# Kernel tuning notes

Measured on AMD Instinct MI355X. Metric: run time of the kernel, lower is better.

Reference implementation:

```python
import jax, jax.numpy as jnp
import numpy as np

EPS = 1e-10


def setup_inputs() -> dict:
    key = jax.random.key(0)
    k1, k2 = jax.random.split(key)
    b, p, c = 8192, 512, 1000
    x = jax.random.normal(k1, (b, p), dtype=jnp.float32)
    means = jax.random.normal(k2, (c, p), dtype=jnp.float32)
    return {"x": x, "means": means}


def reference(x, means):
    # scale factor: L2 norm of the first class mean (np.linalg.norm(mean_logits_np[0]))
    scale = jnp.sqrt(jnp.sum(means[0] ** 2))
    # L2-normalize x along feature dim, then rescale to ||means[0]||
    xn = x / (jnp.linalg.norm(x, axis=1, keepdims=True) + EPS) * scale
    # logits = -||xn - mu_c||^2, expanded as -(||xn||^2 - 2 xn.mu + ||mu||^2)
    # avoids materializing the (b, num_classes, p) intermediate of the original
    x_sq = jnp.sum(xn * xn, axis=1, keepdims=True)          # (b, 1)
    m_sq = jnp.sum(means * means, axis=1)                   # (c,)
    cross = jnp.einsum('bp,cp->bc', xn, means)              # (b, c)
    logits = -(x_sq - 2.0 * cross + m_sq[None, :])
    return logits
```

## Files before the change

kernel.cpp:

```cpp
#include <hip/hip_runtime.h>
#include <hip/hip_bf16.h>
#include <stdint.h>

typedef __bf16 bf16x8 __attribute__((ext_vector_type(8)));
typedef float  f32x4  __attribute__((ext_vector_type(4)));
typedef __attribute__((address_space(1))) const void* gptr_t;
typedef __attribute__((address_space(3))) void*       sptr_t;

#define B_ROWS 8192
#define C_CLS  1000
#define C_PAD  1024
#define P_DIM  512
#define EPS    1e-10f

#define WS_MEANS_BF 0
#define WS_MSQ      1048576
#define WS_XN_BF    1052672
#define WS_XSQ      9441280

__device__ __forceinline__ float dot8(float4 a, float4 b) {
    return a.x * a.x + a.y * a.y + a.z * a.z + a.w * a.w
         + b.x * b.x + b.y * b.y + b.z * b.z + b.w * b.w;
}

__global__ __launch_bounds__(256) void prep_k(const float* __restrict__ x,
                                              const float* __restrict__ means,
                                              __hip_bfloat16* __restrict__ means_bf,
                                              float* __restrict__ m_sq,
                                              __hip_bfloat16* __restrict__ xn_bf,
                                              float* __restrict__ x_sq) {
    const int w = threadIdx.x >> 6;
    const int l = threadIdx.x & 63;
    const int bid = blockIdx.x;

    if (bid < B_ROWS / 4) {
        const int row = bid * 4 + w;
        const float4* m0 = (const float4*)means;
        float4 ma = m0[l * 2];
        float4 mb = m0[l * 2 + 1];
        float ms = dot8(ma, mb);
        const float4* xr = (const float4*)(x + (size_t)row * P_DIM);
        float4 a = xr[l * 2];
        float4 b = xr[l * 2 + 1];
        float s = dot8(a, b);
        #pragma unroll
        for (int off = 32; off > 0; off >>= 1) {
            ms += __shfl_down(ms, off);
            s  += __shfl_down(s, off);
        }
        ms = __shfl(ms, 0);
        s  = __shfl(s, 0);
        float scale = sqrtf(ms);
        float norm  = sqrtf(s);
        float sc    = scale / (norm + EPS);
        alignas(16) __hip_bfloat16 tmp[8];
        tmp[0] = __float2bfloat16(a.x * sc); tmp[1] = __float2bfloat16(a.y * sc);
        tmp[2] = __float2bfloat16(a.z * sc); tmp[3] = __float2bfloat16(a.w * sc);
        tmp[4] = __float2bfloat16(b.x * sc); tmp[5] = __float2bfloat16(b.y * sc);
        tmp[6] = __float2bfloat16(b.z * sc); tmp[7] = __float2bfloat16(b.w * sc);
        *(uint4*)(xn_bf + (size_t)row * P_DIM + l * 8) = *(const uint4*)tmp;
        if (l == 0) {
            float sn = sc * norm;
            x_sq[row] = sn * sn;
        }
    } else {
        const int c = (bid - B_ROWS / 4) * 4 + w;
        if (c < C_CLS) {
            const float4* mr = (const float4*)(means + (size_t)c * P_DIM);
            float4 a = mr[l * 2];
            float4 b = mr[l * 2 + 1];
            float s = dot8(a, b);
            alignas(16) __hip_bfloat16 tmp[8];
            tmp[0] = __float2bfloat16(a.x); tmp[1] = __float2bfloat16(a.y);
            tmp[2] = __float2bfloat16(a.z); tmp[3] = __float2bfloat16(a.w);
            tmp[4] = __float2bfloat16(b.x); tmp[5] = __float2bfloat16(b.y);
            tmp[6] = __float2bfloat16(b.z); tmp[7] = __float2bfloat16(b.w);
            *(uint4*)(means_bf + (size_t)c * P_DIM + l * 8) = *(const uint4*)tmp;
            #pragma unroll
            for (int off = 32; off > 0; off >>= 1) s += __shfl_down(s, off);
            if (l == 0) m_sq[c] = s;
        } else {
            uint4 z = {0u, 0u, 0u, 0u};
            *(uint4*)(means_bf + (size_t)c * P_DIM + l * 8) = z;
            if (l == 0) m_sq[c] = 0.0f;
        }
    }
}

__global__ __launch_bounds__(256, 4) void gemm_k(const __hip_bfloat16* __restrict__ A,
                                                 const __hip_bfloat16* __restrict__ B,
                                                 const float* __restrict__ x_sq,
                                                 const float* __restrict__ m_sq,
                                                 float* __restrict__ out) {
    __shared__ alignas(16) char lds[12288];
    const int t   = threadIdx.x;
    const int w   = t >> 6;
    const int l   = t & 63;
    const int q   = l >> 4;
    const int m16 = l & 15;

    const int brow = blockIdx.y;
    const int bcol = blockIdx.x;

    f32x4 acc[4][2];
    #pragma unroll
    for (int i = 0; i < 4; ++i)
        #pragma unroll
        for (int j = 0; j < 2; ++j) {
            f32x4 z = {0.f, 0.f, 0.f, 0.f};
            acc[i][j] = z;
        }

    const char* Abase = (const char*)A + (size_t)(brow * 64)  * (P_DIM * 2);
    const char* Bbase = (const char*)B + (size_t)(bcol * 128) * (P_DIM * 2);

    for (int k0 = 0; k0 < P_DIM; k0 += 32) {
        #pragma unroll
        for (int r = 0; r < 3; ++r) {
            const int wbase = r * 4096 + w * 1024;
            const int o     = wbase + l * 16;
            const char* g;
            if (r == 0) {
                g = Abase + (size_t)(o >> 6) * (P_DIM * 2) + k0 * 2 + (o & 63);
            } else {
                const int o2 = o - 4096;
                g = Bbase + (size_t)(o2 >> 6) * (P_DIM * 2) + k0 * 2 + (o2 & 63);
            }
            __builtin_amdgcn_global_load_lds((gptr_t)g, (sptr_t)(lds + wbase), 16, 0, 0);
        }
        __syncthreads();

        bf16x8 af[4], bfr[2];
        #pragma unroll
        for (int i = 0; i < 4; ++i) {
            const int m = i * 16 + m16;
            af[i] = *(const bf16x8*)(lds + m * 64 + q * 16);
        }
        #pragma unroll
        for (int j = 0; j < 2; ++j) {
            const int n = w * 32 + j * 16 + m16;
            bfr[j] = *(const bf16x8*)(lds + 4096 + n * 64 + q * 16);
        }
        #pragma unroll
        for (int i = 0; i < 4; ++i)
            #pragma unroll
            for (int j = 0; j < 2; ++j)
                acc[i][j] = __builtin_amdgcn_mfma_f32_16x16x32_bf16(af[i], bfr[j], acc[i][j], 0, 0, 0);
        __syncthreads();
    }

    const int rowbase = brow * 64;
    const int colbase = bcol * 128 + w * 32;
    float msq[2];
    #pragma unroll
    for (int j = 0; j < 2; ++j) {
        const int col = colbase + j * 16 + m16;
        msq[j] = (col < C_CLS) ? m_sq[col] : 0.0f;
    }
    #pragma unroll
    for (int i = 0; i < 4; ++i) {
        #pragma unroll
        for (int reg = 0; reg < 4; ++reg) {
            const int row = rowbase + i * 16 + q * 4 + reg;
            const float xsq = x_sq[row];
            #pragma unroll
            for (int j = 0; j < 2; ++j) {
                const int col = colbase + j * 16 + m16;
                if (col < C_CLS) {
                    out[(size_t)row * C_CLS + col] = 2.0f * acc[i][j][reg] - xsq - msq[j];
                }
            }
        }
    }
}

extern "C" void kernel_launch(void* const* d_in, const int* in_sizes, int n_in,
                              void* d_out, int out_size, void* d_ws, size_t ws_size,
                              hipStream_t stream) {
    const float* x     = (const float*)d_in[0];
    const float* means = (const float*)d_in[1];
    float* out = (float*)d_out;
    char* ws = (char*)d_ws;

    __hip_bfloat16* means_bf = (__hip_bfloat16*)(ws + WS_MEANS_BF);
    float*          m_sq     = (float*)(ws + WS_MSQ);
    __hip_bfloat16* xn_bf    = (__hip_bfloat16*)(ws + WS_XN_BF);
    float*          x_sq     = (float*)(ws + WS_XSQ);

    prep_k<<<B_ROWS / 4 + C_PAD / 4, 256, 0, stream>>>(x, means, means_bf, m_sq, xn_bf, x_sq);
    gemm_k<<<dim3(C_PAD / 128, B_ROWS / 64), 256, 0, stream>>>(xn_bf, means_bf, x_sq, m_sq, out);
}
```

Before: 94.37 us.

## Double K-step per barrier, XOR-swizzle LDS tiles, and remap blocks per XCD

The GEMM now loads 64-wide K slices per iteration instead of 32, which halves the number of barrier pairs and doubles the LDS tile to 24 KB. Each 16-byte chunk is XOR-swizzled by row so that fragment reads from the 128-byte LDS rows avoid bank conflicts. A 1D grid is remapped so blocks landing on the same XCD share A row tiles and improve L2 reuse. The larger LDS footprint may reduce occupancy.

```diff
diff --git a/kernel.cpp b/kernel.cpp
--- a/kernel.cpp
+++ b/kernel.cpp
@@ -92,15 +92,18 @@
                                                  const float* __restrict__ x_sq,
                                                  const float* __restrict__ m_sq,
                                                  float* __restrict__ out) {
-    __shared__ alignas(16) char lds[12288];
+    __shared__ alignas(16) char lds[24576];
     const int t   = threadIdx.x;
     const int w   = t >> 6;
     const int l   = t & 63;
     const int q   = l >> 4;
     const int m16 = l & 15;
 
-    const int brow = blockIdx.y;
-    const int bcol = blockIdx.x;
+    const int n_blk   = blockIdx.x;
+    const int xcd     = n_blk & 7;
+    const int within  = n_blk >> 3;
+    const int brow    = xcd * 16 + (within & 15);
+    const int bcol    = within >> 4;
 
     f32x4 acc[4][2];
     #pragma unroll
@@ -114,38 +117,48 @@
     const char* Abase = (const char*)A + (size_t)(brow * 64)  * (P_DIM * 2);
     const char* Bbase = (const char*)B + (size_t)(bcol * 128) * (P_DIM * 2);
 
-    for (int k0 = 0; k0 < P_DIM; k0 += 32) {
-        #pragma unroll
-        for (int r = 0; r < 3; ++r) {
+    const int swz = (m16 & 7) << 4;
+
+    for (int k0 = 0; k0 < P_DIM; k0 += 64) {
+        #pragma unroll
+        for (int r = 0; r < 6; ++r) {
             const int wbase = r * 4096 + w * 1024;
             const int o     = wbase + l * 16;
             const char* g;
-            if (r == 0) {
-                g = Abase + (size_t)(o >> 6) * (P_DIM * 2) + k0 * 2 + (o & 63);
+            if (r < 2) {
+                const int row = o >> 7;
+                const int c   = (o >> 4) & 7;
+                g = Abase + (size_t)row * (P_DIM * 2) + k0 * 2 + ((c ^ (row & 7)) << 4);
             } else {
-                const int o2 = o - 4096;
-                g = Bbase + (size_t)(o2 >> 6) * (P_DIM * 2) + k0 * 2 + (o2 & 63);
+                const int o2  = o - 8192;
+                const int row = o2 >> 7;
+                const int c   = (o2 >> 4) & 7;
+                g = Bbase + (size_t)row * (P_DIM * 2) + k0 * 2 + ((c ^ (row & 7)) << 4);
             }
             __builtin_amdgcn_global_load_lds((gptr_t)g, (sptr_t)(lds + wbase), 16, 0, 0);
         }
         __syncthreads();
 
-        bf16x8 af[4], bfr[2];
-        #pragma unroll
-        for (int i = 0; i < 4; ++i) {
-            const int m = i * 16 + m16;
-            af[i] = *(const bf16x8*)(lds + m * 64 + q * 16);
-        }
-        #pragma unroll
-        for (int j = 0; j < 2; ++j) {
-            const int n = w * 32 + j * 16 + m16;
-            bfr[j] = *(const bf16x8*)(lds + 4096 + n * 64 + q * 16);
-        }
-        #pragma unroll
-        for (int i = 0; i < 4; ++i)
-            #pragma unroll
-            for (int j = 0; j < 2; ++j)
-                acc[i][j] = __builtin_amdgcn_mfma_f32_16x16x32_bf16(af[i], bfr[j], acc[i][j], 0, 0, 0);
+        #pragma unroll
+        for (int s = 0; s < 2; ++s) {
+            const int kb = s * 64 + q * 16;
+            bf16x8 af[4], bfr[2];
+            #pragma unroll
+            for (int i = 0; i < 4; ++i) {
+                const int m = i * 16 + m16;
+                af[i] = *(const bf16x8*)(lds + m * 128 + (kb ^ swz));
+            }
+            #pragma unroll
+            for (int j = 0; j < 2; ++j) {
+                const int nn = w * 32 + j * 16 + m16;
+                bfr[j] = *(const bf16x8*)(lds + 8192 + nn * 128 + (kb ^ swz));
+            }
+            #pragma unroll
+            for (int i = 0; i < 4; ++i)
+                #pragma unroll
+                for (int j = 0; j < 2; ++j)
+                    acc[i][j] = __builtin_amdgcn_mfma_f32_16x16x32_bf16(af[i], bfr[j], acc[i][j], 0, 0, 0);
+        }
         __syncthreads();
     }
 
@@ -188,5 +201,5 @@
     float*          x_sq     = (float*)(ws + WS_XSQ);
 
     prep_k<<<B_ROWS / 4 + C_PAD / 4, 256, 0, stream>>>(x, means, means_bf, m_sq, xn_bf, x_sq);
-    gemm_k<<<dim3(C_PAD / 128, B_ROWS / 64), 256, 0, stream>>>(xn_bf, means_bf, x_sq, m_sq, out);
-}
+    gemm_k<<<1024, 256, 0, stream>>>(xn_bf, means_bf, x_sq, m_sq, out);
+}
```

Result: faster. 89.32 us (-5.4%).

## Triple-buffer GEMM LDS loads and remap blocks for XCD locality

Applied to the files above, without the earlier changes.

Replaces the load-sync-compute-sync loop with a three-stage LDS ring buffer that prefetches two k-tiles ahead. It uses vmcnt waits and a single barrier per iteration, so global-to-LDS transfers overlap with MFMA work. The 2D grid becomes a 1D grid remapped so that each XCD handles a contiguous band of row blocks, which improves L2 reuse of A. LDS use per block triples, which may reduce occupancy.

```diff
diff --git a/kernel.cpp b/kernel.cpp
--- a/kernel.cpp
+++ b/kernel.cpp
@@ -87,20 +87,38 @@
     }
 }
 
+#define GEMM_STAGE(sbase, k0)                                                              \
+    do {                                                                                   \
+        {                                                          \
+            const int o = w * 1024 + l * 16;                                               \
+            const char* g = Abase + (size_t)(o >> 6) * (P_DIM * 2) + (k0) * 2 + (o & 63);  \
+            __builtin_amdgcn_global_load_lds((gptr_t)g, (sptr_t)(lds + (sbase) + w * 1024), 16, 0, 0); \
+        }                                                                                  \
+        _Pragma("unroll")                                                                  \
+        for (int r = 0; r < 2; ++r) {                             \
+            const int o2 = r * 4096 + w * 1024 + l * 16;                                   \
+            const char* g = Bbase + (size_t)(o2 >> 6) * (P_DIM * 2) + (k0) * 2 + (o2 & 63);\
+            __builtin_amdgcn_global_load_lds((gptr_t)g, (sptr_t)(lds + (sbase) + 4096 + r * 4096 + w * 1024), 16, 0, 0); \
+        }                                                                                  \
+    } while (0)
+
 __global__ __launch_bounds__(256, 4) void gemm_k(const __hip_bfloat16* __restrict__ A,
                                                  const __hip_bfloat16* __restrict__ B,
                                                  const float* __restrict__ x_sq,
                                                  const float* __restrict__ m_sq,
                                                  float* __restrict__ out) {
-    __shared__ alignas(16) char lds[12288];
+    __shared__ alignas(16) char lds[36864];
     const int t   = threadIdx.x;
     const int w   = t >> 6;
     const int l   = t & 63;
     const int q   = l >> 4;
     const int m16 = l & 15;
 
-    const int brow = blockIdx.y;
-    const int bcol = blockIdx.x;
+    const int n_blk  = blockIdx.x;
+    const int xcd    = n_blk & 7;
+    const int within = n_blk >> 3;
+    const int brow   = xcd * 16 + (within & 15);
+    const int bcol   = within >> 4;
 
     f32x4 acc[4][2];
     #pragma unroll
@@ -114,39 +132,44 @@
     const char* Abase = (const char*)A + (size_t)(brow * 64)  * (P_DIM * 2);
     const char* Bbase = (const char*)B + (size_t)(bcol * 128) * (P_DIM * 2);
 
-    for (int k0 = 0; k0 < P_DIM; k0 += 32) {
-        #pragma unroll
-        for (int r = 0; r < 3; ++r) {
-            const int wbase = r * 4096 + w * 1024;
-            const int o     = wbase + l * 16;
-            const char* g;
-            if (r == 0) {
-                g = Abase + (size_t)(o >> 6) * (P_DIM * 2) + k0 * 2 + (o & 63);
-            } else {
-                const int o2 = o - 4096;
-                g = Bbase + (size_t)(o2 >> 6) * (P_DIM * 2) + k0 * 2 + (o2 & 63);
-            }
-            __builtin_amdgcn_global_load_lds((gptr_t)g, (sptr_t)(lds + wbase), 16, 0, 0);
-        }
-        __syncthreads();
-
+    GEMM_STAGE(0, 0);
+    GEMM_STAGE(12288, 32);
+    asm volatile("s_waitcnt vmcnt(3)" ::: "memory");
+    __builtin_amdgcn_s_barrier();
+    asm volatile("" ::: "memory");
+
+    int cur = 0;
+    int stg = 24576;
+
+    for (int kt = 0; kt < 16; ++kt) {
+        if (kt < 14) GEMM_STAGE(stg, (kt + 2) * 32);
+
+        const char* cb = lds + cur;
         bf16x8 af[4], bfr[2];
         #pragma unroll
         for (int i = 0; i < 4; ++i) {
             const int m = i * 16 + m16;
-            af[i] = *(const bf16x8*)(lds + m * 64 + q * 16);
+            af[i] = *(const bf16x8*)(cb + m * 64 + q * 16);
         }
         #pragma unroll
         for (int j = 0; j < 2; ++j) {
-            const int n = w * 32 + j * 16 + m16;
-            bfr[j] = *(const bf16x8*)(lds + 4096 + n * 64 + q * 16);
+            const int nn = w * 32 + j * 16 + m16;
+            bfr[j] = *(const bf16x8*)(cb + 4096 + nn * 64 + q * 16);
         }
         #pragma unroll
         for (int i = 0; i < 4; ++i)
             #pragma unroll
             for (int j = 0; j < 2; ++j)
                 acc[i][j] = __builtin_amdgcn_mfma_f32_16x16x32_bf16(af[i], bfr[j], acc[i][j], 0, 0, 0);
-        __syncthreads();
+
+        if (kt < 15) {
+            if (kt < 14) asm volatile("s_waitcnt vmcnt(3)" ::: "memory");
+            else         asm volatile("s_waitcnt vmcnt(0)" ::: "memory");
+            __builtin_amdgcn_s_barrier();
+            asm volatile("" ::: "memory");
+        }
+        cur = (cur == 24576) ? 0 : cur + 12288;
+        stg = (stg == 24576) ? 0 : stg + 12288;
     }
 
     const int rowbase = brow * 64;
@@ -188,5 +211,5 @@
     float*          x_sq     = (float*)(ws + WS_XSQ);
 
     prep_k<<<B_ROWS / 4 + C_PAD / 4, 256, 0, stream>>>(x, means, means_bf, m_sq, xn_bf, x_sq);
-    gemm_k<<<dim3(C_PAD / 128, B_ROWS / 64), 256, 0, stream>>>(xn_bf, means_bf, x_sq, m_sq, out);
-}
+    gemm_k<<<1024, 256, 0, stream>>>(xn_bf, means_bf, x_sq, m_sq, out);
+}
```

New measurement: 92.70 us. Within noise of the previous version (-1.8%).
